# Optimization experiments

Measured on AMD Instinct MI355X. Metric: run time of the kernel, lower is better.

The kernel has to match this reference:

```python
import jax, jax.numpy as jnp
import numpy as np

B, ID, OD = 4096, 2048, 1024


def _conv_softmax(x, w):
    # x: [..., L]; torch Conv1d(1,1,k=3,stride=1,pad=1,bias=False) then softmax(dim=-1)
    L = x.shape[-1]
    xp = jnp.pad(x, [(0, 0)] * (x.ndim - 1) + [(1, 1)])
    y = w[0] * xp[..., 0:L] + w[1] * xp[..., 1:L + 1] + w[2] * xp[..., 2:L + 2]
    return jax.nn.softmax(y, axis=-1)


def _lstm_cell(x, h, c, Wih, Whh, bih, bhh):
    # torch LSTMCell gate order: i, f, g, o
    g = x @ Wih.T + h @ Whh.T + (bih + bhh)
    i, f, gg, o = jnp.split(g, 4, axis=-1)
    c2 = jax.nn.sigmoid(f) * c + jax.nn.sigmoid(i) * jnp.tanh(gg)
    h2 = jax.nn.sigmoid(o) * jnp.tanh(c2)
    return h2, c2


def _lstm_params(key, in_dim, hid):
    k = 1.0 / np.sqrt(hid)
    ks = jax.random.split(key, 4)
    Wih = jax.random.uniform(ks[0], (4 * hid, in_dim), jnp.float32, -k, k)
    Whh = jax.random.uniform(ks[1], (4 * hid, hid), jnp.float32, -k, k)
    bih = jax.random.uniform(ks[2], (4 * hid,), jnp.float32, -k, k)
    bhh = jax.random.uniform(ks[3], (4 * hid,), jnp.float32, -k, k)
    return Wih, Whh, bih, bhh


def setup_inputs() -> dict:
    key = jax.random.key(0)
    ks = jax.random.split(key, 12)
    spec = jax.random.normal(ks[0], (B, ID), jnp.float32)
    Wih1, Whh1, bih1, bhh1 = _lstm_params(ks[1], ID, OD)
    Wih2, Whh2, bih2, bhh2 = _lstm_params(ks[2], ID // 2, OD // 2)
    Wih3, Whh3, bih3, bhh3 = _lstm_params(ks[3], ID // 4, OD // 4)
    Wih4, Whh4, bih4, bhh4 = _lstm_params(ks[4], ID // 8, OD // 8)
    ck = np.sqrt(1.0 / 3.0)  # Conv1d(1,1,3) init bound
    w2_1h = jax.random.uniform(ks[5], (3,), jnp.float32, -ck, ck)
    w2_1c = jax.random.uniform(ks[6], (3,), jnp.float32, -ck, ck)
    w3_2h = jax.random.uniform(ks[7], (3,), jnp.float32, -ck, ck)
    w3_2c = jax.random.uniform(ks[8], (3,), jnp.float32, -ck, ck)
    w4_3h = jax.random.uniform(ks[9], (3,), jnp.float32, -ck, ck)
    w4_3c = jax.random.uniform(ks[10], (3,), jnp.float32, -ck, ck)
    return dict(spec=spec,
                Wih1=Wih1, Whh1=Whh1, bih1=bih1, bhh1=bhh1,
                Wih2=Wih2, Whh2=Whh2, bih2=bih2, bhh2=bhh2,
                Wih3=Wih3, Whh3=Whh3, bih3=bih3, bhh3=bhh3,
                Wih4=Wih4, Whh4=Whh4, bih4=bih4, bhh4=bhh4,
                w2_1h=w2_1h, w2_1c=w2_1c, w3_2h=w3_2h, w3_2c=w3_2c,
                w4_3h=w4_3h, w4_3c=w4_3c)


def reference(spec, Wih1, Whh1, bih1, bhh1, Wih2, Whh2, bih2, bhh2,
              Wih3, Whh3, bih3, bhh3, Wih4, Whh4, bih4, bhh4,
              w2_1h, w2_1c, w3_2h, w3_2c, w4_3h, w4_3c):
    b = spec.shape[0]
    # Level 4: 8 independent steps, fresh zero state each (torch code passes no hidden)
    x4 = spec.reshape(b, 8, ID // 8)
    z4 = jnp.zeros((b, 8, OD // 8), spec.dtype)
    h4, c4 = _lstm_cell(x4, z4, z4, Wih4, Whh4, bih4, bhh4)   # [b,8,OD/8]
    hb4 = _conv_softmax(h4.reshape(b, 4, OD // 4), w4_3h)      # pairs -> [b,4,OD/4]
    cb4 = _conv_softmax(c4.reshape(b, 4, OD // 4), w4_3c)
    # Level 3: 4 independent steps seeded by level-4 blended states
    x3 = spec.reshape(b, 4, ID // 4)
    h3, c3 = _lstm_cell(x3, hb4, cb4, Wih3, Whh3, bih3, bhh3)  # [b,4,OD/4]
    hb3 = _conv_softmax(h3.reshape(b, 2, OD // 2), w3_2h)      # [b,2,OD/2]
    cb3 = _conv_softmax(c3.reshape(b, 2, OD // 2), w3_2c)
    # Level 2: 2 independent steps
    x2 = spec.reshape(b, 2, ID // 2)
    h2, c2 = _lstm_cell(x2, hb3, cb3, Wih2, Whh2, bih2, bhh2)  # [b,2,OD/2]
    hb2 = _conv_softmax(h2.reshape(b, OD), w2_1h)              # [b,OD]
    cb2 = _conv_softmax(c2.reshape(b, OD), w2_1c)
    # Level 1: single full-resolution step; forward returns out1 = h1
    h1, c1 = _lstm_cell(spec, hb2, cb2, Wih1, Whh1, bih1, bhh1)
    return h1
```

## Files before the change

### kernel.cpp

```cpp
#include <hip/hip_runtime.h>


typedef __bf16 bf16x8 __attribute__((ext_vector_type(8)));
typedef float f32x4 __attribute__((ext_vector_type(4)));
typedef unsigned short u16x4 __attribute__((ext_vector_type(4)));
typedef unsigned short u16x8 __attribute__((ext_vector_type(8)));

#define AS1 __attribute__((address_space(1)))
#define AS3 __attribute__((address_space(3)))

__device__ __forceinline__ unsigned short f2bf(float f) {
    union { float f; unsigned int i; } v; v.f = f;
    unsigned int r = v.i + 0x7fffu + ((v.i >> 16) & 1u);
    return (unsigned short)(r >> 16);
}
__device__ __forceinline__ float bf2f(unsigned short u) {
    union { unsigned int i; float f; } v; v.i = ((unsigned int)u) << 16; return v.f;
}
__device__ __forceinline__ float sigm(float x) { return 1.f / (1.f + __expf(-x)); }
__device__ __forceinline__ float tanh_(float x) { float e = __expf(2.f * x); return 1.f - 2.f / (e + 1.f); }

struct PSeg { const float* src; unsigned short* dst; long g0; int H; int kshift; int dstld; int dstcol; };
struct PArgs {
    PSeg s[7];
    const float* spec; unsigned short* sB;
    const float *bi1, *bh1, *bi2, *bh2, *bi3, *bh3, *bi4, *bh4;
    float *bs1, *bs2, *bs3, *bs4;
};

__global__ __launch_bounds__(256) void prep_all(PArgs pa)
{
    const long NS = 2097152;
    const long NP = 4161536;
    const long total = NS + NP + 7680;
    const long stride = (long)gridDim.x * blockDim.x;
    for (long gi = (long)blockIdx.x * blockDim.x + threadIdx.x; gi < total; gi += stride) {
        if (gi < NS) {
            const float4 v = ((const float4*)pa.spec)[gi];
            u16x4 o; o.x = f2bf(v.x); o.y = f2bf(v.y); o.z = f2bf(v.z); o.w = f2bf(v.w);
            ((u16x4*)pa.sB)[gi] = o;
        } else if (gi < NS + NP) {
            const long gp = gi - NS;
            int si = 0;
#pragma unroll
            for (int k = 1; k < 7; ++k) si += (gp >= pa.s[k].g0);
            const PSeg sg = pa.s[si];
            const long i = gp - sg.g0;
            const int kq = 1 << sg.kshift;
            const int p = (int)(i >> sg.kshift);
            const int kk = ((int)i & (kq - 1)) << 2;
            const int o = ((p >> 6) << 4) | (p & 15);
            const int q = (p >> 4) & 3;
            const long r = (long)q * sg.H + o;
            const float4 v = *(const float4*)(sg.src + (r << (sg.kshift + 2)) + kk);
            u16x4 wv; wv.x = f2bf(v.x); wv.y = f2bf(v.y); wv.z = f2bf(v.z); wv.w = f2bf(v.w);
            *(u16x4*)(sg.dst + (long)p * sg.dstld + sg.dstcol + kk) = wv;
        } else {
            const int i = (int)(gi - NS - NP);
            const float *bih, *bhh; float* dst; int H, j;
            if (i < 4096)      { bih = pa.bi1; bhh = pa.bh1; dst = pa.bs1; H = 1024; j = i; }
            else if (i < 6144) { bih = pa.bi2; bhh = pa.bh2; dst = pa.bs2; H = 512;  j = i - 4096; }
            else if (i < 7168) { bih = pa.bi3; bhh = pa.bh3; dst = pa.bs3; H = 256;  j = i - 6144; }
            else               { bih = pa.bi4; bhh = pa.bh4; dst = pa.bs4; H = 128;  j = i - 7168; }
            const int o = ((j >> 6) << 4) | (j & 15);
            const int q = (j >> 4) & 3;
            dst[j] = bih[q * H + o] + bhh[q * H + o];
        }
    }
}

#define QUAD(AF, S, NS_, BF)                                                                \
    { _Pragma("unroll") for (int mi = 0; mi < 4; ++mi) {                                    \
        _Pragma("unroll") for (int ni = 0; ni < 2; ++ni) {                                  \
            acc[(S)*4+mi][(NS_)*2+ni] = __builtin_amdgcn_mfma_f32_16x16x32_bf16(            \
                AF[mi][0], BF[ni][0], acc[(S)*4+mi][(NS_)*2+ni], 0, 0, 0);                  \
            acc[(S)*4+mi][(NS_)*2+ni] = __builtin_amdgcn_mfma_f32_16x16x32_bf16(            \
                AF[mi][1], BF[ni][1], acc[(S)*4+mi][(NS_)*2+ni], 0, 0, 0);                  \
    } } }

#define GLL(gsrc, loff) __builtin_amdgcn_global_load_lds(                                   \
    (const AS1 void*)(gsrc), (AS3 void*)(lds + (loff)), 16, 0, 0)

#define FENCE asm volatile("" ::: "memory")

#define STAGE_A(tts, qq)                                                                    \
    { if ((tts) < nk0) {                                                                    \
        const size_t ko = (size_t)(tts) * 64;                                               \
        GLL(A0 + a0off0 + ko, ((qq) << 16) + sd0);                                          \
        GLL(A0 + a0off1 + ko, ((qq) << 16) + sd1);                                          \
        GLL(A0 + a0off0 + k128_0 + ko, ((qq) << 16) + 16384 + sd0);                         \
        GLL(A0 + a0off1 + k128_0 + ko, ((qq) << 16) + 16384 + sd1);                         \
    } else {                                                                                \
        const size_t ko = (size_t)((tts) - nk0) * 64;                                       \
        GLL(A1 + a1off0 + ko, ((qq) << 16) + sd0);                                          \
        GLL(A1 + a1off1 + ko, ((qq) << 16) + sd1);                                          \
        GLL(A1 + a1off0 + k128_1 + ko, ((qq) << 16) + 16384 + sd0);                         \
        GLL(A1 + a1off1 + k128_1 + ko, ((qq) << 16) + 16384 + sd1);                         \
    } }

template<bool HAS_CIN, bool LAST>
__global__ __launch_bounds__(512, 2) void gemm8(
    const unsigned short* __restrict__ A0, const unsigned short* __restrict__ A1,
    const int K0, const int K1,
    const unsigned short* __restrict__ W,
    const float* __restrict__ bsum, const unsigned short* __restrict__ Cin,
    float* __restrict__ HoutF, unsigned short* __restrict__ HoutB,
    unsigned short* __restrict__ CoutB, const int H)
{
    __shared__ __align__(16) char lds[131072];
    const int t = threadIdx.x;
    const int w = t >> 6, l = t & 63;
    const int wr = w >> 2, wc = w & 3;
    const int K = K0 + K1;
    const int nk0 = K0 >> 6;

    const int GX = gridDim.x, GY = gridDim.y;
    const int nwg = GX * GY;
    const int bid = (int)blockIdx.y * GX + (int)blockIdx.x;
    const int swz = (bid & 7) * (nwg >> 3) + (bid >> 3);
    const int m0 = (swz / GY) * 256, n0 = (swz % GY) * 256;

    const int colsw = ((l & 7) ^ (l >> 3)) * 8;
    const int arow = m0 + w * 16 + (l >> 3);
    const size_t a0off0 = (size_t)arow * K0 + colsw;
    const size_t a0off1 = a0off0 + (size_t)8 * K0;
    const size_t a1off0 = (size_t)arow * K1 + colsw;
    const size_t a1off1 = a1off0 + (size_t)8 * K1;
    const size_t k128_0 = (size_t)128 * K0;
    const size_t k128_1 = (size_t)128 * K1;
    const size_t k128 = (size_t)128 * K;
    const size_t boff0 = (size_t)(n0 + w * 16 + (l >> 3)) * K + colsw;
    const size_t boff1 = boff0 + (size_t)8 * K;
    const int sd0 = w * 2048 + l * 16;
    const int sd1 = sd0 + 1024;

    const int lr128 = (l & 15) * 128;
    const int sw0 = (((l >> 4)    ) ^ (l & 7)) * 16;
    const int sw1 = (((l >> 4) + 4) ^ (l & 7)) * 16;

    f32x4 acc[8][4];
#pragma unroll
    for (int i = 0; i < 8; ++i)
#pragma unroll
        for (int j = 0; j < 4; ++j) acc[i][j] = (f32x4){0.f, 0.f, 0.f, 0.f};

    const int NT = K >> 6;

    STAGE_A(0, 0);
    GLL(W + boff0, 32768 + sd0);              GLL(W + boff1, 32768 + sd1);
    GLL(W + boff0 + k128, 49152 + sd0);       GLL(W + boff1 + k128, 49152 + sd1);
    GLL(W + boff0 + 64, 98304 + sd0);         GLL(W + boff1 + 64, 98304 + sd1);
    GLL(W + boff0 + k128 + 64, 114688 + sd0); GLL(W + boff1 + k128 + 64, 114688 + sd1);

    bf16x8 aLo[4][2], aHi[4][2], bF0[2][2], bF1[2][2];

    for (int tt = 0; tt < NT; ++tt) {
        const int q = tt & 1, qn = q ^ 1;
        const int rbA = (q << 16) + (wr << 14) + lr128;
        const int rbB = (q << 16) + 32768 + wc * 8192 + lr128;
        const bool st1 = (tt + 1 < NT), st2 = (tt + 2 < NT);

        if (st1) { asm volatile("s_waitcnt vmcnt(4)" ::: "memory"); }
        else     { asm volatile("s_waitcnt vmcnt(0)" ::: "memory"); }
        __builtin_amdgcn_s_barrier();
        FENCE;

#pragma unroll
        for (int mi = 0; mi < 4; ++mi) {
            aLo[mi][0] = *(const bf16x8*)(lds + rbA + mi * 2048 + sw0);
            aLo[mi][1] = *(const bf16x8*)(lds + rbA + mi * 2048 + sw1);
        }
#pragma unroll
        for (int ni = 0; ni < 2; ++ni) {
            bF0[ni][0] = *(const bf16x8*)(lds + rbB + ni * 2048 + sw0);
            bF0[ni][1] = *(const bf16x8*)(lds + rbB + ni * 2048 + sw1);
            bF1[ni][0] = *(const bf16x8*)(lds + rbB + 4096 + ni * 2048 + sw0);
            bF1[ni][1] = *(const bf16x8*)(lds + rbB + 4096 + ni * 2048 + sw1);
        }
        if (st1) { STAGE_A(tt + 1, qn); }
#pragma unroll
        for (int mi = 0; mi < 4; ++mi) {
            aHi[mi][0] = *(const bf16x8*)(lds + rbA + 8192 + mi * 2048 + sw0);
            aHi[mi][1] = *(const bf16x8*)(lds + rbA + 8192 + mi * 2048 + sw1);
        }

        __builtin_amdgcn_s_setprio(1);
        QUAD(aLo, 0, 0, bF0);
        QUAD(aLo, 0, 1, bF1);
        __builtin_amdgcn_s_setprio(0);
        __builtin_amdgcn_s_barrier();
        FENCE;

        if (st2) {
            const size_t ko2 = (size_t)(tt + 2) * 64;
            GLL(W + boff0 + ko2, (q << 16) + 32768 + sd0);
            GLL(W + boff1 + ko2, (q << 16) + 32768 + sd1);
            GLL(W + boff0 + k128 + ko2, (q << 16) + 49152 + sd0);
            GLL(W + boff1 + k128 + ko2, (q << 16) + 49152 + sd1);
        }
        __builtin_amdgcn_s_setprio(1);
        QUAD(aHi, 1, 1, bF1);
        QUAD(aHi, 1, 0, bF0);
        __builtin_amdgcn_s_setprio(0);
    }

    const int ocol = (n0 >> 6) * 16 + wc * 16 + (l & 15);
    const int bb = n0 + wc * 64 + (l & 15);
    const float b0 = bsum[bb], b1 = bsum[bb + 16], b2 = bsum[bb + 32], b3 = bsum[bb + 48];
    const int mrow0 = m0 + wr * 128 + (l >> 4) * 4;
#pragma unroll
    for (int mi = 0; mi < 8; ++mi)
#pragma unroll
        for (int j = 0; j < 4; ++j) {
            const size_t m = (size_t)(mrow0 + mi * 16 + j);
            const float gi = acc[mi][0][j] + b0;
            const float gf = acc[mi][1][j] + b1;
            const float gg = acc[mi][2][j] + b2;
            const float go = acc[mi][3][j] + b3;
            float c2 = sigm(gi) * tanh_(gg);
            if (HAS_CIN) c2 += sigm(gf) * bf2f(Cin[m * H + ocol]);
            const float h2 = sigm(go) * tanh_(c2);
            if (LAST) {
                HoutF[m * H + ocol] = h2;
            } else {
                HoutB[m * H + ocol] = f2bf(h2);
                CoutB[m * H + ocol] = f2bf(c2);
            }
        }
}

template<int L>
__global__ __launch_bounds__(256) void conv_dual(
    const unsigned short* __restrict__ Hin, const unsigned short* __restrict__ Cin,
    const float* __restrict__ w3h, const float* __restrict__ w3c,
    unsigned short* __restrict__ hbuf, unsigned short* __restrict__ cbuf)
{
    constexpr int R = 2048 / L;
    constexpr int TPR = L / 8;
    __shared__ float xs[R][L + 2];
    __shared__ float red[8];
    const int nb = gridDim.x >> 1;
    const bool isC = (int)blockIdx.x >= nb;
    const int row0 = (isC ? (int)blockIdx.x - nb : (int)blockIdx.x) * R;
    const unsigned short* Xs = isC ? Cin : Hin;
    const float* w3 = isC ? w3c : w3h;
    const int t = threadIdx.x;
    const int r = t / TPR;
    const int c8 = (t % TPR) * 8;
    const float w0 = w3[0], w1 = w3[1], w2 = w3[2];

    const u16x8 v = *(const u16x8*)(Xs + (size_t)(row0 + r) * L + c8);
#pragma unroll
    for (int k = 0; k < 8; ++k) xs[r][c8 + 1 + k] = bf2f(v[k]);
    if (t < R) { xs[t][0] = 0.f; xs[t][L + 1] = 0.f; }
    __syncthreads();

    float y[8];
    float vmax = -3.4e38f;
#pragma unroll
    for (int k = 0; k < 8; ++k) {
        y[k] = w0 * xs[r][c8 + k] + w1 * xs[r][c8 + k + 1] + w2 * xs[r][c8 + k + 2];
        vmax = fmaxf(vmax, y[k]);
    }
#pragma unroll
    for (int off = (TPR >= 64 ? 32 : TPR / 2); off >= 1; off >>= 1)
        vmax = fmaxf(vmax, __shfl_xor(vmax, off));
    if (TPR == 128) {
        if ((t & 63) == 0) red[t >> 6] = vmax;
        __syncthreads();
        vmax = fmaxf(red[2 * r], red[2 * r + 1]);
    }
    float s = 0.f;
#pragma unroll
    for (int k = 0; k < 8; ++k) { y[k] = __expf(y[k] - vmax); s += y[k]; }
#pragma unroll
    for (int off = (TPR >= 64 ? 32 : TPR / 2); off >= 1; off >>= 1)
        s += __shfl_xor(s, off);
    if (TPR == 128) {
        if ((t & 63) == 0) red[4 + (t >> 6)] = s;
        __syncthreads();
        s = red[4 + 2 * r] + red[4 + 2 * r + 1];
    }
    const float inv = 1.f / s;
    u16x8 o;
#pragma unroll
    for (int k = 0; k < 8; ++k) o[k] = f2bf(y[k] * inv);
    if (isC) *(u16x8*)(cbuf + (size_t)(row0 + r) * L + c8) = o;
    else     *(u16x8*)(hbuf + (size_t)(row0 + r) * L + c8) = o;
}

extern "C" void kernel_launch(void* const* d_in, const int* in_sizes, int n_in,
                              void* d_out, int out_size, void* d_ws, size_t ws_size,
                              hipStream_t stream)
{
    (void)in_sizes; (void)n_in; (void)out_size; (void)ws_size;
    const float* spec  = (const float*)d_in[0];
    const float* Wih1  = (const float*)d_in[1];
    const float* Whh1  = (const float*)d_in[2];
    const float* bih1  = (const float*)d_in[3];
    const float* bhh1  = (const float*)d_in[4];
    const float* Wih2  = (const float*)d_in[5];
    const float* Whh2  = (const float*)d_in[6];
    const float* bih2  = (const float*)d_in[7];
    const float* bhh2  = (const float*)d_in[8];
    const float* Wih3  = (const float*)d_in[9];
    const float* Whh3  = (const float*)d_in[10];
    const float* bih3  = (const float*)d_in[11];
    const float* bhh3  = (const float*)d_in[12];
    const float* Wih4  = (const float*)d_in[13];
    const float* bih4  = (const float*)d_in[15];
    const float* bhh4  = (const float*)d_in[16];
    const float* w2_1h = (const float*)d_in[17];
    const float* w2_1c = (const float*)d_in[18];
    const float* w3_2h = (const float*)d_in[19];
    const float* w3_2c = (const float*)d_in[20];
    const float* w4_3h = (const float*)d_in[21];
    const float* w4_3c = (const float*)d_in[22];

    char* ws = (char*)d_ws;
    unsigned short* h   = (unsigned short*)(ws + 0);
    unsigned short* c   = (unsigned short*)(ws + (size_t)8388608);
    unsigned short* cb  = (unsigned short*)(ws + (size_t)16777216);
    unsigned short* hb  = (unsigned short*)(ws + (size_t)25165824);
    unsigned short* sB  = (unsigned short*)(ws + (size_t)33554432);
    unsigned short* Wc1 = (unsigned short*)(ws + (size_t)50331648);
    unsigned short* Wc2 = (unsigned short*)(ws + (size_t)75497472);
    unsigned short* Wc3 = (unsigned short*)(ws + (size_t)81788928);
    unsigned short* W4  = (unsigned short*)(ws + (size_t)83361792);
    float*          bs1 = (float*)(ws + (size_t)83623936);
    float*          bs2 = bs1 + 4096;
    float*          bs3 = bs2 + 4096;
    float*          bs4 = bs3 + 4096;

    PArgs pa;
    pa.s[0] = { Wih1, Wc1,       0, 1024, 9, 3072,    0 };
    pa.s[1] = { Whh1, Wc1, 2097152, 1024, 8, 3072, 2048 };
    pa.s[2] = { Wih2, Wc2, 3145728,  512, 8, 1536,    0 };
    pa.s[3] = { Whh2, Wc2, 3670016,  512, 7, 1536, 1024 };
    pa.s[4] = { Wih3, Wc3, 3932160,  256, 7,  768,    0 };
    pa.s[5] = { Whh3, Wc3, 4063232,  256, 6,  768,  512 };
    pa.s[6] = { Wih4, W4,  4128768,  128, 6,  256,    0 };
    pa.spec = spec; pa.sB = sB;
    pa.bi1 = bih1; pa.bh1 = bhh1; pa.bi2 = bih2; pa.bh2 = bhh2;
    pa.bi3 = bih3; pa.bh3 = bhh3; pa.bi4 = bih4; pa.bh4 = bhh4;
    pa.bs1 = bs1; pa.bs2 = bs2; pa.bs3 = bs3; pa.bs4 = bs4;
    prep_all<<<2048, 256, 0, stream>>>(pa);

    gemm8<false, false><<<dim3(128, 2), 512, 0, stream>>>(
        sB, nullptr, 256, 0, W4, bs4, nullptr, nullptr, h, c, 128);
    conv_dual<256><<<4096, 256, 0, stream>>>(h, c, w4_3h, w4_3c, hb, cb);

    gemm8<true, false><<<dim3(64, 4), 512, 0, stream>>>(
        sB, hb, 512, 256, Wc3, bs3, cb, nullptr, h, c, 256);
    conv_dual<512><<<4096, 256, 0, stream>>>(h, c, w3_2h, w3_2c, hb, cb);

    gemm8<true, false><<<dim3(32, 8), 512, 0, stream>>>(
        sB, hb, 1024, 512, Wc2, bs2, cb, nullptr, h, c, 512);
    conv_dual<1024><<<4096, 256, 0, stream>>>(h, c, w2_1h, w2_1c, hb, cb);

    gemm8<true, true><<<dim3(16, 16), 512, 0, stream>>>(
        sB, hb, 2048, 1024, Wc1, bs1, cb, (float*)d_out, nullptr, nullptr, 1024);
}
```

Before: 271.4 us.

## Shrink GEMM tile to 128x128 with 4 waves for more workgroups

Reworks the fused LSTM gate GEMM from a 256x256 tile with 8 waves and 128KB of LDS to a 128x128 tile with 4 waves and 64KB of LDS. The A and B staging loads, wave layout, MFMA clusters and epilogue indexing are all rewritten to match, and the grids are quadrupled. The aim is to fill all compute units with more workgroups (the old grids had only 256 blocks) and to allow more blocks resident per CU. In exchange, operand reuse per tile drops, so each output needs more global and LDS traffic.

```diff
diff --git a/kernel.cpp b/kernel.cpp
--- a/kernel.cpp
+++ b/kernel.cpp
@@ -69,15 +69,6 @@
     }
 }
 
-#define QUAD(AF, S, NS_, BF)                                                                \
-    { _Pragma("unroll") for (int mi = 0; mi < 4; ++mi) {                                    \
-        _Pragma("unroll") for (int ni = 0; ni < 2; ++ni) {                                  \
-            acc[(S)*4+mi][(NS_)*2+ni] = __builtin_amdgcn_mfma_f32_16x16x32_bf16(            \
-                AF[mi][0], BF[ni][0], acc[(S)*4+mi][(NS_)*2+ni], 0, 0, 0);                  \
-            acc[(S)*4+mi][(NS_)*2+ni] = __builtin_amdgcn_mfma_f32_16x16x32_bf16(            \
-                AF[mi][1], BF[ni][1], acc[(S)*4+mi][(NS_)*2+ni], 0, 0, 0);                  \
-    } } }
-
 #define GLL(gsrc, loff) __builtin_amdgcn_global_load_lds(                                   \
     (const AS1 void*)(gsrc), (AS3 void*)(lds + (loff)), 16, 0, 0)
 
@@ -86,20 +77,40 @@
 #define STAGE_A(tts, qq)                                                                    \
     { if ((tts) < nk0) {                                                                    \
         const size_t ko = (size_t)(tts) * 64;                                               \
-        GLL(A0 + a0off0 + ko, ((qq) << 16) + sd0);                                          \
-        GLL(A0 + a0off1 + ko, ((qq) << 16) + sd1);                                          \
-        GLL(A0 + a0off0 + k128_0 + ko, ((qq) << 16) + 16384 + sd0);                         \
-        GLL(A0 + a0off1 + k128_0 + ko, ((qq) << 16) + 16384 + sd1);                         \
+        GLL(A0 + a0off + ko,                   ((qq) << 15) + sd);                          \
+        GLL(A0 + a0off + (size_t)32*K0 + ko,   ((qq) << 15) + 4096 + sd);                   \
+        GLL(A0 + a0off + (size_t)64*K0 + ko,   ((qq) << 15) + 8192 + sd);                   \
+        GLL(A0 + a0off + (size_t)96*K0 + ko,   ((qq) << 15) + 12288 + sd);                  \
     } else {                                                                                \
         const size_t ko = (size_t)((tts) - nk0) * 64;                                       \
-        GLL(A1 + a1off0 + ko, ((qq) << 16) + sd0);                                          \
-        GLL(A1 + a1off1 + ko, ((qq) << 16) + sd1);                                          \
-        GLL(A1 + a1off0 + k128_1 + ko, ((qq) << 16) + 16384 + sd0);                         \
-        GLL(A1 + a1off1 + k128_1 + ko, ((qq) << 16) + 16384 + sd1);                         \
+        GLL(A1 + a1off + ko,                   ((qq) << 15) + sd);                          \
+        GLL(A1 + a1off + (size_t)32*K1 + ko,   ((qq) << 15) + 4096 + sd);                   \
+        GLL(A1 + a1off + (size_t)64*K1 + ko,   ((qq) << 15) + 8192 + sd);                   \
+        GLL(A1 + a1off + (size_t)96*K1 + ko,   ((qq) << 15) + 12288 + sd);                  \
     } }
 
+#define STAGE_B(tts, qq)                                                                    \
+    { const size_t ko = (size_t)(tts) * 64;                                                 \
+        GLL(W + boff + ko,                   ((qq) << 15) + 16384 + sd);                    \
+        GLL(W + boff + (size_t)32*K + ko,    ((qq) << 15) + 20480 + sd);                    \
+        GLL(W + boff + (size_t)64*K + ko,    ((qq) << 15) + 24576 + sd);                    \
+        GLL(W + boff + (size_t)96*K + ko,    ((qq) << 15) + 28672 + sd); }
+
+#define CLUSTER(MI, AF)                                                                     \
+    { _Pragma("unroll") for (int mi = 0; mi < 2; ++mi) {                                    \
+        _Pragma("unroll") for (int ni = 0; ni < 2; ++ni) {                                  \
+            acc[(MI)+mi][ni] = __builtin_amdgcn_mfma_f32_16x16x32_bf16(                     \
+                AF[mi][0], bF0[ni][0], acc[(MI)+mi][ni], 0, 0, 0);                          \
+            acc[(MI)+mi][ni] = __builtin_amdgcn_mfma_f32_16x16x32_bf16(                     \
+                AF[mi][1], bF0[ni][1], acc[(MI)+mi][ni], 0, 0, 0);                          \
+            acc[(MI)+mi][ni+2] = __builtin_amdgcn_mfma_f32_16x16x32_bf16(                   \
+                AF[mi][0], bF1[ni][0], acc[(MI)+mi][ni+2], 0, 0, 0);                        \
+            acc[(MI)+mi][ni+2] = __builtin_amdgcn_mfma_f32_16x16x32_bf16(                   \
+                AF[mi][1], bF1[ni][1], acc[(MI)+mi][ni+2], 0, 0, 0);                        \
+    } } }
+
 template<bool HAS_CIN, bool LAST>
-__global__ __launch_bounds__(512, 2) void gemm8(
+__global__ __launch_bounds__(256, 2) void gemm8(
     const unsigned short* __restrict__ A0, const unsigned short* __restrict__ A1,
     const int K0, const int K1,
     const unsigned short* __restrict__ W,
@@ -107,10 +118,10 @@
     float* __restrict__ HoutF, unsigned short* __restrict__ HoutB,
     unsigned short* __restrict__ CoutB, const int H)
 {
-    __shared__ __align__(16) char lds[131072];
+    __shared__ __align__(16) char lds[65536];
     const int t = threadIdx.x;
     const int w = t >> 6, l = t & 63;
-    const int wr = w >> 2, wc = w & 3;
+    const int wr = w >> 1, wc = w & 1;
     const int K = K0 + K1;
     const int nk0 = K0 >> 6;
 
@@ -118,46 +129,36 @@
     const int nwg = GX * GY;
     const int bid = (int)blockIdx.y * GX + (int)blockIdx.x;
     const int swz = (bid & 7) * (nwg >> 3) + (bid >> 3);
-    const int m0 = (swz / GY) * 256, n0 = (swz % GY) * 256;
-
-    const int colsw = ((l & 7) ^ (l >> 3)) * 8;
-    const int arow = m0 + w * 16 + (l >> 3);
-    const size_t a0off0 = (size_t)arow * K0 + colsw;
-    const size_t a0off1 = a0off0 + (size_t)8 * K0;
-    const size_t a1off0 = (size_t)arow * K1 + colsw;
-    const size_t a1off1 = a1off0 + (size_t)8 * K1;
-    const size_t k128_0 = (size_t)128 * K0;
-    const size_t k128_1 = (size_t)128 * K1;
-    const size_t k128 = (size_t)128 * K;
-    const size_t boff0 = (size_t)(n0 + w * 16 + (l >> 3)) * K + colsw;
-    const size_t boff1 = boff0 + (size_t)8 * K;
-    const int sd0 = w * 2048 + l * 16;
-    const int sd1 = sd0 + 1024;
+    const int m0 = (swz / GY) * 128, n0 = (swz % GY) * 128;
+
+    const int colsw = ((t & 7) ^ ((t >> 3) & 7)) * 8;
+    const size_t a0off = (size_t)(m0 + (t >> 3)) * K0 + colsw;
+    const size_t a1off = (size_t)(m0 + (t >> 3)) * K1 + colsw;
+    const size_t boff  = (size_t)(n0 + (t >> 3)) * K  + colsw;
+    const int sd = t * 16;
 
     const int lr128 = (l & 15) * 128;
     const int sw0 = (((l >> 4)    ) ^ (l & 7)) * 16;
     const int sw1 = (((l >> 4) + 4) ^ (l & 7)) * 16;
 
-    f32x4 acc[8][4];
-#pragma unroll
-    for (int i = 0; i < 8; ++i)
+    f32x4 acc[4][4];
+#pragma unroll
+    for (int i = 0; i < 4; ++i)
 #pragma unroll
         for (int j = 0; j < 4; ++j) acc[i][j] = (f32x4){0.f, 0.f, 0.f, 0.f};
 
     const int NT = K >> 6;
 
     STAGE_A(0, 0);
-    GLL(W + boff0, 32768 + sd0);              GLL(W + boff1, 32768 + sd1);
-    GLL(W + boff0 + k128, 49152 + sd0);       GLL(W + boff1 + k128, 49152 + sd1);
-    GLL(W + boff0 + 64, 98304 + sd0);         GLL(W + boff1 + 64, 98304 + sd1);
-    GLL(W + boff0 + k128 + 64, 114688 + sd0); GLL(W + boff1 + k128 + 64, 114688 + sd1);
-
-    bf16x8 aLo[4][2], aHi[4][2], bF0[2][2], bF1[2][2];
+    STAGE_B(0, 0);
+    STAGE_B(1, 1);
+
+    bf16x8 aLo[2][2], aHi[2][2], bF0[2][2], bF1[2][2];
 
     for (int tt = 0; tt < NT; ++tt) {
         const int q = tt & 1, qn = q ^ 1;
-        const int rbA = (q << 16) + (wr << 14) + lr128;
-        const int rbB = (q << 16) + 32768 + wc * 8192 + lr128;
+        const int rbA = (q << 15) + wr * 8192 + lr128;
+        const int rbB = (q << 15) + 16384 + wc * 8192 + lr128;
         const bool st1 = (tt + 1 < NT), st2 = (tt + 2 < NT);
 
         if (st1) { asm volatile("s_waitcnt vmcnt(4)" ::: "memory"); }
@@ -166,7 +167,7 @@
         FENCE;
 
 #pragma unroll
-        for (int mi = 0; mi < 4; ++mi) {
+        for (int mi = 0; mi < 2; ++mi) {
             aLo[mi][0] = *(const bf16x8*)(lds + rbA + mi * 2048 + sw0);
             aLo[mi][1] = *(const bf16x8*)(lds + rbA + mi * 2048 + sw1);
         }
@@ -179,37 +180,29 @@
         }
         if (st1) { STAGE_A(tt + 1, qn); }
 #pragma unroll
-        for (int mi = 0; mi < 4; ++mi) {
-            aHi[mi][0] = *(const bf16x8*)(lds + rbA + 8192 + mi * 2048 + sw0);
-            aHi[mi][1] = *(const bf16x8*)(lds + rbA + 8192 + mi * 2048 + sw1);
+        for (int mi = 0; mi < 2; ++mi) {
+            aHi[mi][0] = *(const bf16x8*)(lds + rbA + 4096 + mi * 2048 + sw0);
+            aHi[mi][1] = *(const bf16x8*)(lds + rbA + 4096 + mi * 2048 + sw1);
         }
 
         __builtin_amdgcn_s_setprio(1);
-        QUAD(aLo, 0, 0, bF0);
-        QUAD(aLo, 0, 1, bF1);
+        CLUSTER(0, aLo);
         __builtin_amdgcn_s_setprio(0);
         __builtin_amdgcn_s_barrier();
         FENCE;
 
-        if (st2) {
-            const size_t ko2 = (size_t)(tt + 2) * 64;
-            GLL(W + boff0 + ko2, (q << 16) + 32768 + sd0);
-            GLL(W + boff1 + ko2, (q << 16) + 32768 + sd1);
-            GLL(W + boff0 + k128 + ko2, (q << 16) + 49152 + sd0);
-            GLL(W + boff1 + k128 + ko2, (q << 16) + 49152 + sd1);
-        }
+        if (st2) { STAGE_B(tt + 2, q); }
         __builtin_amdgcn_s_setprio(1);
-        QUAD(aHi, 1, 1, bF1);
-        QUAD(aHi, 1, 0, bF0);
+        CLUSTER(2, aHi);
         __builtin_amdgcn_s_setprio(0);
     }
 
     const int ocol = (n0 >> 6) * 16 + wc * 16 + (l & 15);
     const int bb = n0 + wc * 64 + (l & 15);
     const float b0 = bsum[bb], b1 = bsum[bb + 16], b2 = bsum[bb + 32], b3 = bsum[bb + 48];
-    const int mrow0 = m0 + wr * 128 + (l >> 4) * 4;
-#pragma unroll
-    for (int mi = 0; mi < 8; ++mi)
+    const int mrow0 = m0 + wr * 64 + (l >> 4) * 4;
+#pragma unroll
+    for (int mi = 0; mi < 4; ++mi)
 #pragma unroll
         for (int j = 0; j < 4; ++j) {
             const size_t m = (size_t)(mrow0 + mi * 16 + j);
@@ -346,18 +339,18 @@
     pa.bs1 = bs1; pa.bs2 = bs2; pa.bs3 = bs3; pa.bs4 = bs4;
     prep_all<<<2048, 256, 0, stream>>>(pa);
 
-    gemm8<false, false><<<dim3(128, 2), 512, 0, stream>>>(
+    gemm8<false, false><<<dim3(256, 4), 256, 0, stream>>>(
         sB, nullptr, 256, 0, W4, bs4, nullptr, nullptr, h, c, 128);
     conv_dual<256><<<4096, 256, 0, stream>>>(h, c, w4_3h, w4_3c, hb, cb);
 
-    gemm8<true, false><<<dim3(64, 4), 512, 0, stream>>>(
+    gemm8<true, false><<<dim3(128, 8), 256, 0, stream>>>(
         sB, hb, 512, 256, Wc3, bs3, cb, nullptr, h, c, 256);
     conv_dual<512><<<4096, 256, 0, stream>>>(h, c, w3_2h, w3_2c, hb, cb);
 
-    gemm8<true, false><<<dim3(32, 8), 512, 0, stream>>>(
+    gemm8<true, false><<<dim3(64, 16), 256, 0, stream>>>(
         sB, hb, 1024, 512, Wc2, bs2, cb, nullptr, h, c, 512);
     conv_dual<1024><<<4096, 256, 0, stream>>>(h, c, w2_1h, w2_1c, hb, cb);
 
-    gemm8<true, true><<<dim3(16, 16), 512, 0, stream>>>(
+    gemm8<true, true><<<dim3(32, 32), 256, 0, stream>>>(
         sB, hb, 2048, 1024, Wc1, bs1, cb, (float*)d_out, nullptr, nullptr, 1024);
 }
```

Measured after the change: 301.6 us. 1.11x slower.
